# Optimization experiments

Measured on AMD Instinct MI355X. Metric: run time of the kernel, lower is better.

## Reference

```python
import jax, jax.numpy as jnp
import numpy as np

EPS = 1e-6

def _ln(x, g, b):
    m = jnp.mean(x, -1, keepdims=True)
    v = jnp.mean((x - m) ** 2, -1, keepdims=True)
    return (x - m) * jax.lax.rsqrt(v + 1e-5) * g + b

def _mha(qin, kin, vin, wq, bq, wk, bk, wv, bv, wo, bo, nh=8):
    B, T, D = qin.shape
    S = kin.shape[1]
    dh = D // nh
    q = (qin @ wq + bq).reshape(B, T, nh, dh)
    k = (kin @ wk + bk).reshape(B, S, nh, dh)
    v = (vin @ wv + bv).reshape(B, S, nh, dh)
    a = jax.nn.softmax(jnp.einsum('bthd,bshd->bhts', q, k) / np.float32(np.sqrt(dh)), -1)
    o = jnp.einsum('bhts,bshd->bthd', a, v).reshape(B, T, D)
    return o @ wo + bo

def _sinu_pe(pos, num_feats=128, temperature=20.0):
    # pos: [..., 2] (x, y); returns [..., 2*num_feats] ordered (y-feats, x-feats)
    dim_t = temperature ** ((2 * (jnp.arange(num_feats) // 2)) / num_feats)
    e = pos[..., None] * (2 * np.pi) / dim_t  # [..., 2, F]
    e = jnp.stack([jnp.sin(e[..., 0::2]), jnp.cos(e[..., 1::2])], -1).reshape(e.shape)
    return jnp.concatenate([e[..., 1, :], e[..., 0, :]], -1)

def _spatial36(b1, b2, sizes):
    # b1, b2: [B, Q, 4]; sizes: [B, 2] = (h, w). UPT-style 18 feats + log -> 36.
    h = sizes[:, 0:1]; w = sizes[:, 1:2]
    c1x = (b1[..., 0] + b1[..., 2]) / 2; c1y = (b1[..., 1] + b1[..., 3]) / 2
    c2x = (b2[..., 0] + b2[..., 2]) / 2; c2y = (b2[..., 1] + b2[..., 3]) / 2
    w1 = b1[..., 2] - b1[..., 0]; h1 = b1[..., 3] - b1[..., 1]
    w2 = b2[..., 2] - b2[..., 0]; h2 = b2[..., 3] - b2[..., 1]
    a1 = w1 * h1; a2 = w2 * h2
    dx = jnp.abs(c2x - c1x) / (w1 + EPS)
    dy = jnp.abs(c2y - c1y) / (h1 + EPS)
    ix = jnp.clip(jnp.minimum(b1[..., 2], b2[..., 2]) - jnp.maximum(b1[..., 0], b2[..., 0]), 0)
    iy = jnp.clip(jnp.minimum(b1[..., 3], b2[..., 3]) - jnp.maximum(b1[..., 1], b2[..., 1]), 0)
    inter = ix * iy
    iou = inter / (a1 + a2 - inter + EPS)
    f = jnp.stack([c1x / w, c1y / h, c2x / w, c2y / h, w1 / w, h1 / h, w2 / w, h2 / h,
                   a1 / (h * w), a2 / (h * w), a2 / (a1 + EPS), w1 / (h1 + EPS), w2 / (h2 + EPS), iou,
                   (c2x > c1x) * dx, (c2x < c1x) * dx, (c2y > c1y) * dy, (c2y < c1y) * dy], -1)
    return jnp.concatenate([f, jnp.log(f + EPS)], -1)

def _forward(boxes, embeds, image_sizes, pose, line, sw1, sb1, sw2, sb2, sw3, sb3, bw, bb, pw, pb, lw, lb, enc_pe_w, enc_pe_b, enc_qkv_w, enc_qkv_b, enc_out_w, enc_out_b, enc_ff1_w, enc_ff1_b, enc_ff2_w, enc_ff2_b, enc_ln1_g, enc_ln1_b, enc_ln2_g, enc_ln2_b, dec_q_w, dec_q_b, dec_kv_w, dec_kv_b, dec_out_w, dec_out_b, dec_ff1_w, dec_ff1_b, dec_ff2_w, dec_ff2_b, dec_ln1_g, dec_ln1_b, dec_ln2_g, dec_ln2_b, fc1_w, fc1_b, fc2_w, fc2_b, mln1_g, mln1_b, mln2_g, mln2_b, m1_w, m1_b, m2_w, m2_b, labels, nh):
    B, N, _ = boxes.shape
    # static human-object pairing (x != y) & (x < nh)
    xg, yg = np.meshgrid(np.arange(N), np.arange(N), indexing='ij')
    keep = (xg != yg) & (xg < nh)
    xk = jnp.asarray(xg[keep]); yk = jnp.asarray(yg[keep])  # [P]
    # line features: adaptive-avg-pool(1,1) + 1x1 conv == spatial mean + linear
    line_feat = jnp.mean(line, axis=(2, 3)) @ lw + lb  # [B, 256]
    # spatial head on all N*N ordered pairs, then gather kept pairs
    xa = jnp.asarray(xg.reshape(-1)); ya = jnp.asarray(yg.reshape(-1))
    f36 = _spatial36(boxes[:, xa], boxes[:, ya], image_sizes)  # [B, N*N, 36]
    s = jax.nn.relu(f36 @ sw1 + sb1)
    s = jax.nn.relu(s @ sw2 + sb2)
    s = jax.nn.relu(s @ sw3 + sb3)
    spa = s.reshape(B, N, N, -1)[:, xk, yk]  # [B, P, R]
    # box sinusoidal positional encodings (cat of centre-PE and wh-PE)
    whwh = image_sizes[:, jnp.array([1, 0, 1, 0])][:, None]  # [B,1,4]
    bxn = boxes / whwh
    ctr = (bxn[..., :2] + bxn[..., 2:]) / 2
    whb = bxn[..., 2:] - bxn[..., :2]
    box_pe = jnp.concatenate([_sinu_pe(ctr), _sinu_pe(whb)], -1)  # [B, N, 512]
    # 2-layer transformer encoder over instance tokens (pos added to q,k)
    posx = box_pe @ enc_pe_w + enc_pe_b
    x = embeds
    for i in range(enc_qkv_w.shape[0]):
        wq, wk_, wv = jnp.split(enc_qkv_w[i], 3, axis=1)
        bq, bk_, bv = jnp.split(enc_qkv_b[i], 3)
        qk = x + posx
        att = _mha(qk, qk, x, wq, bq, wk_, bk_, wv, bv, enc_out_w[i], enc_out_b[i])
        x = _ln(x + att, enc_ln1_g[i], enc_ln1_b[i])
        ff = jax.nn.relu(x @ enc_ff1_w[i] + enc_ff1_b[i]) @ enc_ff2_w[i] + enc_ff2_b[i]
        x = _ln(x + ff, enc_ln2_g[i], enc_ln2_b[i])
    # pair gather + human/object positional embeds (box PE projected + line feature)
    pe_h = box_pe[:, xk] @ bw + bb + line_feat[:, None, :]
    pe_o = box_pe[:, yk] @ bw + bb + line_feat[:, None, :]
    h = x[:, xk]; o = x[:, yk]  # [B, P, 256]
    pose_ctx = pose @ pw + pb  # [B, M, 256]
    # HO refine decoder: cross-attention from pair tokens to pose tokens
    for l in range(dec_q_w.shape[0]):
        wk_, wv = jnp.split(dec_kv_w[l], 2, axis=1)
        bk_, bv = jnp.split(dec_kv_b[l], 2)
        def _layer(feat, pe):
            att = _mha(feat + pe, pose_ctx, pose_ctx, dec_q_w[l], dec_q_b[l], wk_, bk_, wv, bv, dec_out_w[l], dec_out_b[l])
            feat = _ln(feat + att, dec_ln1_g[l], dec_ln1_b[l])
            ff = jax.nn.relu(feat @ dec_ff1_w[l] + dec_ff1_b[l]) @ dec_ff2_w[l] + dec_ff2_b[l]
            return _ln(feat + ff, dec_ln2_g[l], dec_ln2_b[l])
        h = _layer(h, pe_h)
        o = _layer(o, pe_o)
    # multi-modal fusion
    ho = jnp.concatenate([h, o], -1)  # [B, P, 512]
    ho = _ln(ho @ fc1_w + fc1_b, mln1_g, mln1_b)
    sp = _ln(spa @ fc2_w + fc2_b, mln2_g, mln2_b)
    z = jax.nn.relu(jnp.concatenate([ho, sp], -1))
    z = jax.nn.relu(z @ m1_w + m1_b)
    z = jax.nn.relu(z @ m2_w + m2_b)
    return z  # [B, P, 256] HOI query features

def setup_inputs() -> dict:
    key = jax.random.key(0)
    ks = iter(jax.random.split(key, 80))
    B, N, NH, M, HH, WW = 16, 128, 32, 64, 8, 8
    W = 0.05
    def rn(shape, s=1.0):
        return jax.random.normal(next(ks), shape, dtype=jnp.float32) * s
    def ru(shape):
        return jax.random.uniform(next(ks), shape, dtype=jnp.float32)
    sizes = 800.0 + 480.0 * ru((B, 2))  # (h, w)
    wh = sizes[:, jnp.array([1, 0])]
    xy = ru((B, N, 2)) * wh[:, None] * 0.7
    bwh = ru((B, N, 2)) * wh[:, None] * 0.25 + 4.0
    boxes = jnp.concatenate([xy, xy + bwh], -1)
    labels = jnp.concatenate([jnp.zeros((B, NH), jnp.int32), jax.random.randint(next(ks), (B, N - NH), 1, 81, dtype=jnp.int32)], -1)
    return dict(
        boxes=boxes, embeds=rn((B, N, 256)), image_sizes=sizes, pose=rn((B, M, 768)), line=rn((B, 2048, HH, WW)),
        sw1=rn((36, 128), W), sb1=jnp.zeros((128,)), sw2=rn((128, 256), W), sb2=jnp.zeros((256,)), sw3=rn((256, 256), W), sb3=jnp.zeros((256,)),
        bw=rn((512, 256), W), bb=jnp.zeros((256,)), pw=rn((768, 256), W), pb=jnp.zeros((256,)), lw=rn((2048, 256), W), lb=jnp.zeros((256,)),
        enc_pe_w=rn((512, 256), W), enc_pe_b=jnp.zeros((256,)),
        enc_qkv_w=rn((2, 256, 768), W), enc_qkv_b=jnp.zeros((2, 768)), enc_out_w=rn((2, 256, 256), W), enc_out_b=jnp.zeros((2, 256)),
        enc_ff1_w=rn((2, 256, 1024), W), enc_ff1_b=jnp.zeros((2, 1024)), enc_ff2_w=rn((2, 1024, 256), W), enc_ff2_b=jnp.zeros((2, 256)),
        enc_ln1_g=jnp.ones((2, 256)), enc_ln1_b=jnp.zeros((2, 256)), enc_ln2_g=jnp.ones((2, 256)), enc_ln2_b=jnp.zeros((2, 256)),
        dec_q_w=rn((2, 256, 256), W), dec_q_b=jnp.zeros((2, 256)), dec_kv_w=rn((2, 256, 512), W), dec_kv_b=jnp.zeros((2, 512)),
        dec_out_w=rn((2, 256, 256), W), dec_out_b=jnp.zeros((2, 256)),
        dec_ff1_w=rn((2, 256, 1024), W), dec_ff1_b=jnp.zeros((2, 1024)), dec_ff2_w=rn((2, 1024, 256), W), dec_ff2_b=jnp.zeros((2, 256)),
        dec_ln1_g=jnp.ones((2, 256)), dec_ln1_b=jnp.zeros((2, 256)), dec_ln2_g=jnp.ones((2, 256)), dec_ln2_b=jnp.zeros((2, 256)),
        fc1_w=rn((512, 256), W), fc1_b=jnp.zeros((256,)), fc2_w=rn((256, 256), W), fc2_b=jnp.zeros((256,)),
        mln1_g=jnp.ones((256,)), mln1_b=jnp.zeros((256,)), mln2_g=jnp.ones((256,)), mln2_b=jnp.zeros((256,)),
        m1_w=rn((512, 384), W), m1_b=jnp.zeros((384,)), m2_w=rn((384, 256), W), m2_b=jnp.zeros((256,)),
        labels=labels, nh=NH)

def reference(boxes, embeds, image_sizes, pose, line, sw1, sb1, sw2, sb2, sw3, sb3, bw, bb, pw, pb, lw, lb, enc_pe_w, enc_pe_b, enc_qkv_w, enc_qkv_b, enc_out_w, enc_out_b, enc_ff1_w, enc_ff1_b, enc_ff2_w, enc_ff2_b, enc_ln1_g, enc_ln1_b, enc_ln2_g, enc_ln2_b, dec_q_w, dec_q_b, dec_kv_w, dec_kv_b, dec_out_w, dec_out_b, dec_ff1_w, dec_ff1_b, dec_ff2_w, dec_ff2_b, dec_ln1_g, dec_ln1_b, dec_ln2_g, dec_ln2_b, fc1_w, fc1_b, fc2_w, fc2_b, mln1_g, mln1_b, mln2_g, mln2_b, m1_w, m1_b, m2_w, m2_b, labels, nh):
    return _forward(boxes, embeds, image_sizes, pose, line, sw1, sb1, sw2, sb2, sw3, sb3, bw, bb, pw, pb, lw, lb, enc_pe_w, enc_pe_b, enc_qkv_w, enc_qkv_b, enc_out_w, enc_out_b, enc_ff1_w, enc_ff1_b, enc_ff2_w, enc_ff2_b, enc_ln1_g, enc_ln1_b, enc_ln2_g, enc_ln2_b, dec_q_w, dec_q_b, dec_kv_w, dec_kv_b, dec_out_w, dec_out_b, dec_ff1_w, dec_ff1_b, dec_ff2_w, dec_ff2_b, dec_ln1_g, dec_ln1_b, dec_ln2_g, dec_ln2_b, fc1_w, fc1_b, fc2_w, fc2_b, mln1_g, mln1_b, mln2_g, mln2_b, m1_w, m1_b, m2_w, m2_b, labels, nh)
```

## Files before the change

kernel.cpp:

```cpp
#include <hip/hip_runtime.h>
#include <stdint.h>

static constexpr int B      = 16;
static constexpr int N      = 128;
static constexpr int P      = 4064;
static constexpr int MPOSE  = 64;
static constexpr int64_t BN = (int64_t)B * N;
static constexpr int64_t BP = (int64_t)B * P;

#define TWO_PI 6.283185307179586f
#define QSCALE 0.17677669529663687f

typedef __attribute__((ext_vector_type(4))) float f32x4;
typedef __attribute__((ext_vector_type(8))) short bf16x8;
typedef __attribute__((ext_vector_type(8))) unsigned short u16x8;
typedef __attribute__((ext_vector_type(4))) unsigned short u16x4;

__device__ __forceinline__ unsigned short f2bf(float f) {
    union { float f; unsigned u; } v; v.f = f;
    unsigned r = (v.u + 0x7fffu + ((v.u >> 16) & 1u)) >> 16;
    return (unsigned short)r;
}
__device__ __forceinline__ float bf2f(unsigned short u) {
    union { unsigned u; float f; } v; v.u = (unsigned)u << 16;
    return v.f;
}
__device__ __forceinline__ void pair_xy(int p, int& x, int& y) {
    x = p / 127;
    int r = p - x * 127;
    y = (r < x) ? r : r + 1;
}
__device__ __forceinline__ int xcd_swz(int orig, int nwg) {
    int q = nwg >> 3, r = nwg & 7;
    int xcd = orig & 7, idx = orig >> 3;
// ... 3 lines not shown
    __builtin_amdgcn_global_load_lds(
        (const __attribute__((address_space(1))) void*)g,
        (__attribute__((address_space(3))) void*)l, 16, 0, 0);
}

struct WDesc { const float* src; int64_t dstOff; int K, Nn, Kpad, blockStart; };
struct WTable { WDesc d[29]; int nDesc; };

__global__ __launch_bounds__(256) void wprep_all_k(WTable t, unsigned short* __restrict__ wt)
{
    __shared__ float s[32][33];
    int bid = blockIdx.x;
    int di = 0;
    for (int i = 1; i < t.nDesc; ++i) if (t.d[i].blockStart <= bid) di = i;
    const WDesc& d = t.d[di];
    int lbid = bid - d.blockStart;
    int kTiles = d.Kpad >> 5;
    int k0 = (lbid % kTiles) * 32, n0 = (lbid / kTiles) * 32;
    int tx = threadIdx.x & 31, ty = threadIdx.x >> 5;
#pragma unroll
    for (int i = 0; i < 4; ++i) {
        int k = k0 + ty + i * 8;
        s[ty + i * 8][tx] = (k < d.K) ? d.src[(int64_t)k * d.Nn + n0 + tx] : 0.f;
    }
    __syncthreads();
    unsigned short* dst = wt + d.dstOff;
#pragma unroll
    for (int i = 0; i < 4; ++i) {
        int n = n0 + ty + i * 8;
        dst[(int64_t)n * d.Kpad + k0 + tx] = f2bf(s[tx][ty + i * 8]);
    }
}

template <bool RELU_OUT>
__global__ __launch_bounds__(256) void bgemm_k(
    const float* __restrict__ A, const float* __restrict__ A2, int lda,
    const unsigned short* __restrict__ Bt, int ldk,
    const float* __restrict__ bias,
    const float* __restrict__ Cadd, int addLd,
    const float* __restrict__ lfp,
    float* __restrict__ C, int ldc,
    int kSteps)
{
    __shared__ unsigned short As[128][40];
    __shared__ unsigned short Bs[128][40];
    const int tid  = threadIdx.x;
    const int lane = tid & 63;
    const int wave = tid >> 6;
    const int wr = wave >> 1, wc = wave & 1;
    const int row0 = blockIdx.y * 128, col0 = blockIdx.x * 128;
    const int l15 = lane & 15, l4 = lane >> 4;
    const int sr = tid >> 1;
    const int sh = (tid & 1) * 16;

    f32x4 acc[4][4] = {};

    for (int ks = 0; ks < kSteps; ++ks) {
        const int k0 = ks * 32;
        {
            const int64_t off = (int64_t)(row0 + sr) * lda + k0 + sh;
            const float* ap = A + off;
            float v[16];
#pragma unroll
            for (int i = 0; i < 4; ++i) {
                float4 tv = ((const float4*)ap)[i];
                v[i*4+0] = tv.x; v[i*4+1] = tv.y; v[i*4+2] = tv.z; v[i*4+3] = tv.w;
            }
            if (A2) {
                const float* ap2 = A2 + off;
#pragma unroll
                for (int i = 0; i < 4; ++i) {
                    float4 tv = ((const float4*)ap2)[i];
                    v[i*4+0] += tv.x; v[i*4+1] += tv.y; v[i*4+2] += tv.z; v[i*4+3] += tv.w;
                }
            }
            u16x8 p0, p1;
#pragma unroll
            for (int j = 0; j < 8; ++j) { p0[j] = f2bf(v[j]); p1[j] = f2bf(v[8 + j]); }
            *(u16x8*)&As[sr][sh]     = p0;
            *(u16x8*)&As[sr][sh + 8] = p1;
        }
        {
            const unsigned short* bp = Bt + (int64_t)(col0 + sr) * ldk + k0 + sh;
            *(u16x8*)&Bs[sr][sh]     = *(const u16x8*)bp;
            *(u16x8*)&Bs[sr][sh + 8] = *(const u16x8*)(bp + 8);
        }
        __syncthreads();
        bf16x8 af[4], bfr[4];
#pragma unroll
        for (int f = 0; f < 4; ++f) {
            af[f]  = *(const bf16x8*)&As[wr * 64 + f * 16 + l15][l4 * 8];
            bfr[f] = *(const bf16x8*)&Bs[wc * 64 + f * 16 + l15][l4 * 8];
        }
#pragma unroll
        for (int i = 0; i < 4; ++i)
#pragma unroll
            for (int j = 0; j < 4; ++j)
                acc[i][j] = __builtin_amdgcn_mfma_f32_16x16x32_bf16(af[i], bfr[j], acc[i][j], 0, 0, 0);
        __syncthreads();
    }
#pragma unroll
    for (int i = 0; i < 4; ++i) {
        int rb = row0 + wr * 64 + i * 16 + l4 * 4;
#pragma unroll
        for (int j = 0; j < 4; ++j) {
            int c = col0 + wc * 64 + j * 16 + l15;
            float bv = bias ? bias[c] : 0.f;
#pragma unroll
            for (int e = 0; e < 4; ++e) {
                int r = rb + e;
                float vv = acc[i][j][e] + bv;
                if (Cadd && c < addLd) vv += Cadd[(int64_t)r * addLd + c];
                if (lfp) vv += lfp[(r >> 7) * 256 + c];
                if (RELU_OUT) vv = fmaxf(vv, 0.f);
                C[(int64_t)r * ldc + c] = vv;
            }
        }
    }
}

static void bgemm(hipStream_t st,
                  const float* A, const float* A2, int lda,
                  const unsigned short* Bt, int ldk, const float* bias,
                  const float* Cadd, int addLd, const float* lfp,
                  float* C, int ldc, int M, int Ncols, int K, bool reluOut)
{
    dim3 g(Ncols / 128, M / 128), b(256);
    if (reluOut) bgemm_k<true><<<g,b,0,st>>>(A,A2,lda,Bt,ldk,bias,Cadd,addLd,lfp,C,ldc,K/32);
    else         bgemm_k<false><<<g,b,0,st>>>(A,A2,lda,Bt,ldk,bias,Cadd,addLd,lfp,C,ldc,K/32);
}

__global__ __launch_bounds__(256) void tgemm_k(
    const float* __restrict__ A, int lda,
    const unsigned short* __restrict__ Bt, int ldk,
    const float* __restrict__ bias,
    const float* __restrict__ res,
    const float* __restrict__ g, const float* __restrict__ be,
    float* __restrict__ C, int kSteps)
{
    __shared__ unsigned short As[64][40];
    __shared__ unsigned short Bs[256][40];
    __shared__ float partS[64][4], partQ[64][4];
    __shared__ float statM[64], statI[64];
    const int tid = threadIdx.x;
    const int lane = tid & 63, w = tid >> 6;
    const int l15 = lane & 15, l4 = lane >> 4;
    const int row0 = blockIdx.x * 64;
    const int sra = tid >> 2, sha = (tid & 3) * 8;

    f32x4 acc[4][4] = {};
    for (int ks = 0; ks < kSteps; ++ks) {
        int k0 = ks * 32;
        {
            const float* ap = A + (int64_t)(row0 + sra) * lda + k0 + sha;
            float4 t0 = ((const float4*)ap)[0];
            float4 t1 = ((const float4*)ap)[1];
            u16x8 p;
            p[0]=f2bf(t0.x); p[1]=f2bf(t0.y); p[2]=f2bf(t0.z); p[3]=f2bf(t0.w);
            p[4]=f2bf(t1.x); p[5]=f2bf(t1.y); p[6]=f2bf(t1.z); p[7]=f2bf(t1.w);
            *(u16x8*)&As[sra][sha] = p;
        }
        {
            const unsigned short* bp = Bt + (int64_t)tid * ldk + k0;
#pragma unroll
            for (int q = 0; q < 4; ++q)
                *(u16x8*)&Bs[tid][q * 8] = *(const u16x8*)(bp + q * 8);
        }
        __syncthreads();
        bf16x8 af[4], bfr[4];
#pragma unroll
        for (int f = 0; f < 4; ++f) {
            af[f]  = *(const bf16x8*)&As[f * 16 + l15][l4 * 8];
            bfr[f] = *(const bf16x8*)&Bs[w * 64 + f * 16 + l15][l4 * 8];
        }
#pragma unroll
        for (int i = 0; i < 4; ++i)
#pragma unroll
            for (int j = 0; j < 4; ++j)
                acc[i][j] = __builtin_amdgcn_mfma_f32_16x16x32_bf16(af[i], bfr[j], acc[i][j], 0, 0, 0);
        __syncthreads();
// ... 24 lines not shown
        }
    }
    if (l15 == 0) {
#pragma unroll
        for (int i = 0; i < 4; ++i)
#pragma unroll
        for (int e = 0; e < 4; ++e) {
            int r = i * 16 + l4 * 4 + e;
            partS[r][w] = ps[i][e];
            partQ[r][w] = pq[i][e];
        }
    }
    __syncthreads();
    if (tid < 64) {
        float s = partS[tid][0] + partS[tid][1] + partS[tid][2] + partS[tid][3];
        float q = partQ[tid][0] + partQ[tid][1] + partQ[tid][2] + partQ[tid][3];
        float m = s * (1.f/256.f);
        float var = q * (1.f/256.f) - m * m;
        statM[tid] = m;
        statI[tid] = rsqrtf(var + 1e-5f);
    }
    __syncthreads();
#pragma unroll
    for (int i = 0; i < 4; ++i)
#pragma unroll
    for (int j = 0; j < 4; ++j) {
        int c = w * 64 + j * 16 + l15;
#pragma unroll
        for (int e = 0; e < 4; ++e) {
            int r = i * 16 + l4 * 4 + e;
            C[(int64_t)(row0 + r) * 256 + c] = (acc[i][j][e] - statM[r]) * statI[r] * g[c] + be[c];
        }
    }
}

template <bool RELU_OUT, bool OUT_BF16>
__global__ __launch_bounds__(256) void hgemm_k(
    const unsigned short* __restrict__ A, int lda,
    const unsigned short* __restrict__ Bt, int ldk,
    const float* __restrict__ bias,
    void* __restrict__ Cv, int ldc,
    int kSteps, int nx)
{
    __shared__ unsigned short As[128][32];
    __shared__ unsigned short Bs[128][32];
    const int tid  = threadIdx.x;
    const int lane = tid & 63;
    const int wave = tid >> 6;
    const int wr = wave >> 1, wc = wave & 1;
    const int wgid = xcd_swz(blockIdx.x, gridDim.x);
    const int row0 = (wgid / nx) * 128, col0 = (wgid % nx) * 128;
    const int l15 = lane & 15, l4 = lane >> 4;
    const int srow = lane >> 2;
    const int scol = (lane & 3) * 8;

    f32x4 acc[4][4] = {};

    for (int ks = 0; ks < kSteps; ++ks) {
        const int k0 = ks * 32;
#pragma unroll
        for (int i = 0; i < 2; ++i) {
            int seg = wave * 2 + i;
            int r = seg * 16 + srow;
            gld16(A  + (int64_t)(row0 + r) * lda + k0 + scol, &As[seg * 16][0]);
            gld16(Bt + (int64_t)(col0 + r) * ldk + k0 + scol, &Bs[seg * 16][0]);
        }
        __syncthreads();
        bf16x8 af[4], bfr[4];
#pragma unroll
        for (int f = 0; f < 4; ++f) {
            af[f]  = *(const bf16x8*)&As[wr * 64 + f * 16 + l15][l4 * 8];
            bfr[f] = *(const bf16x8*)&Bs[wc * 64 + f * 16 + l15][l4 * 8];
        }
#pragma unroll
        for (int i = 0; i < 4; ++i)
#pragma unroll
            for (int j = 0; j < 4; ++j)
                acc[i][j] = __builtin_amdgcn_mfma_f32_16x16x32_bf16(af[i], bfr[j], acc[i][j], 0, 0, 0);
        __syncthreads();
    }
#pragma unroll
    for (int i = 0; i < 4; ++i) {
        int rb = row0 + wr * 64 + i * 16 + l4 * 4;
#pragma unroll
        for (int j = 0; j < 4; ++j) {
            int c = col0 + wc * 64 + j * 16 + l15;
            float bv = bias ? bias[c] : 0.f;
#pragma unroll
            for (int e = 0; e < 4; ++e) {
                int64_t off = (int64_t)(rb + e) * ldc + c;
// ... 224 lines not shown
#pragma unroll 4
    for (int k = 0; k < 256; ++k) acc += lmb[k] * lwp[(int64_t)k * 256];
    red[cc][jj] = acc;
    __syncthreads();
    if (cc == 0) {
        float s = lb[j];
#pragma unroll
        for (int i = 0; i < 8; ++i) s += red[i][jj];
        lf[b * 256 + j] = s;
    }
}

__global__ __launch_bounds__(512) void boxpe_k(
    const float* __restrict__ boxes, const float* __restrict__ sizes, float* __restrict__ boxpe)
{
    int row = blockIdx.x;
    int b = row >> 7;
    int i = threadIdx.x;
    const float* bx = boxes + (int64_t)row * 4;
    float h = sizes[b * 2 + 0], w = sizes[b * 2 + 1];
    float x0 = bx[0] / w, y0 = bx[1] / h, x1 = bx[2] / w, y1 = bx[3] / h;
    int seg = i >> 7, j = i & 127, k = j >> 1;
    float val;
    switch (seg) {
        case 0: val = (y0 + y1) * 0.5f; break;
        case 1: val = (x0 + x1) * 0.5f; break;
        case 2: val = (y1 - y0); break;
        default: val = (x1 - x0); break;
    }
    float dimt = exp2f((float)k * (4.321928094887362f / 64.f));
    float arg = val * TWO_PI / dimt;
    boxpe[(int64_t)row * 512 + i] = (j & 1) ? cosf(arg) : sinf(arg);
}

__global__ __launch_bounds__(128) void enc_attn_k(
    const float* __restrict__ qkv, float* __restrict__ outp)
{
    int b = blockIdx.x >> 3, hd = blockIdx.x & 7;
    __shared__ float kl[128][32];
    __shared__ float vl[128][32];
    int tid = threadIdx.x;
    for (int i = tid; i < 128 * 32; i += 128) {
        int s = i >> 5, j = i & 31;
        const float* rp = qkv + ((int64_t)(b * 128 + s)) * 768 + hd * 32 + j;
        kl[s][j] = rp[256];
        vl[s][j] = rp[512];
    }
    __syncthreads();
    int t = tid;
    const float* qp = qkv + ((int64_t)(b * 128 + t)) * 768 + hd * 32;
    float qr[32];
#pragma unroll
    for (int j = 0; j < 32; ++j) qr[j] = qp[j] * QSCALE;
    float m = -1e30f, l = 0.f;
    for (int s = 0; s < 128; ++s) {
        float d = 0.f;
#pragma unroll
        for (int j = 0; j < 32; ++j) d += qr[j] * kl[s][j];
        float mn = fmaxf(m, d);
        l = l * __expf(m - mn) + __expf(d - mn);
        m = mn;
    }
    float acc[32] = {};
    for (int s = 0; s < 128; ++s) {
        float d = 0.f;
#pragma unroll
        for (int j = 0; j < 32; ++j) d += qr[j] * kl[s][j];
        float wgt = __expf(d - m);
#pragma unroll
        for (int j = 0; j < 32; ++j) acc[j] += wgt * vl[s][j];
    }
    float linv = 1.f / l;
    float* op = outp + ((int64_t)(b * 128 + t)) * 256 + hd * 32;
#pragma unroll
    for (int j = 0; j < 32; ++j) op[j] = acc[j] * linv;
}

__global__ __launch_bounds__(256) void dec_attn_k(
    const float* __restrict__ q, const float* __restrict__ kv,
    float* __restrict__ outp, int rows, int rpb)
{
    int hd = blockIdx.y;
    int r0 = blockIdx.x * 256;
    __shared__ float kl[2][64][32];
    __shared__ float vl[2][64][32];
    int tid = threadIdx.x;
    int b0 = r0 / rpb;
    int b1 = (r0 + 255) / rpb;
    if (b1 >= B) b1 = B - 1;
    for (int i = tid; i < 64 * 32; i += 256) {
        int s = i >> 5, j = i & 31;
        int64_t off0 = ((int64_t)(b0 * MPOSE + s)) * 512 + hd * 32 + j;
        int64_t off1 = ((int64_t)(b1 * MPOSE + s)) * 512 + hd * 32 + j;
        kl[0][s][j] = kv[off0];
        vl[0][s][j] = kv[off0 + 256];
        kl[1][s][j] = kv[off1];
        vl[1][s][j] = kv[off1 + 256];
    }
    __syncthreads();
    int r = r0 + tid;
    if (r >= rows) return;
    int which = (r / rpb == b0) ? 0 : 1;
    int64_t qoff = (int64_t)r * 256 + hd * 32;
    float qr[32];
#pragma unroll
    for (int j = 0; j < 32; ++j) qr[j] = q[qoff + j] * QSCALE;
    float m = -1e30f, l = 0.f;
    for (int s = 0; s < 64; ++s) {
        float d = 0.f;
#pragma unroll
        for (int j = 0; j < 32; ++j) d += qr[j] * kl[which][s][j];
        float mn = fmaxf(m, d);
        l = l * __expf(m - mn) + __expf(d - mn);
        m = mn;
    }
    float acc[32] = {};
    for (int s = 0; s < 64; ++s) {
        float d = 0.f;
#pragma unroll
        for (int j = 0; j < 32; ++j) d += qr[j] * kl[which][s][j];
        float wgt = __expf(d - m);
#pragma unroll
        for (int j = 0; j < 32; ++j) acc[j] += wgt * vl[which][s][j];
    }
    float linv = 1.f / l;
#pragma unroll
    for (int j = 0; j < 32; ++j) outp[qoff + j] = acc[j] * linv;
}

static constexpr int64_t WT_QKV  = 0;
static constexpr int64_t WT_EOUT = WT_QKV  + 2*196608;
static constexpr int64_t WT_EFF1 = WT_EOUT + 2*65536;
static constexpr int64_t WT_EFF2 = WT_EFF1 + 2*262144;
static constexpr int64_t WT_DQ   = WT_EFF2 + 2*262144;
static constexpr int64_t WT_DKV  = WT_DQ   + 2*65536;
static constexpr int64_t WT_DOUT = WT_DKV  + 2*131072;
static constexpr int64_t WT_DFF1 = WT_DOUT + 2*65536;
static constexpr int64_t WT_DFF2 = WT_DFF1 + 2*262144;
static constexpr int64_t WT_SW1  = WT_DFF2 + 2*262144;
static constexpr int64_t WT_SW2  = WT_SW1 + 8192;
static constexpr int64_t WT_SW3  = WT_SW2 + 32768;
static constexpr int64_t WT_BW   = WT_SW3 + 65536;
static constexpr int64_t WT_PW   = WT_BW  + 131072;
static constexpr int64_t WT_EPE  = WT_PW  + 196608;
static constexpr int64_t WT_FC1  = WT_EPE + 131072;
static constexpr int64_t WT_FC2  = WT_FC1 + 131072;
static constexpr int64_t WT_M1   = WT_FC2 + 65536;
static constexpr int64_t WT_M2   = WT_M1  + 196608;
static constexpr int64_t WT_TOTAL = WT_M2 + 98304;

extern "C" void kernel_launch(void* const* d_in, const int* in_sizes, int n_in,
                              void* d_out, int out_size, void* d_ws, size_t ws_size,
                              hipStream_t stream)
{
    (void)in_sizes; (void)n_in; (void)out_size;
    const float* boxes     = (const float*)d_in[0];
    const float* embeds    = (const float*)d_in[1];
    const float* sizes     = (const float*)d_in[2];
    const float* pose      = (const float*)d_in[3];
    const float* line      = (const float*)d_in[4];
    const float* sw1 = (const float*)d_in[5];  const float* sb1 = (const float*)d_in[6];
    const float* sw2 = (const float*)d_in[7];  const float* sb2 = (const float*)d_in[8];
    const float* sw3 = (const float*)d_in[9];  const float* sb3 = (const float*)d_in[10];
    const float* bw  = (const float*)d_in[11]; const float* bb  = (const float*)d_in[12];
    const float* pw  = (const float*)d_in[13]; const float* pb  = (const float*)d_in[14];
    const float* lw  = (const float*)d_in[15]; const float* lb  = (const float*)d_in[16];
    const float* enc_pe_w  = (const float*)d_in[17]; const float* enc_pe_b = (const float*)d_in[18];
    const float* enc_qkv_w = (const float*)d_in[19]; const float* enc_qkv_b = (const float*)d_in[20];
    const float* enc_out_w = (const float*)d_in[21]; const float* enc_out_b = (const float*)d_in[22];
    const float* enc_ff1_w = (const float*)d_in[23]; const float* enc_ff1_b = (const float*)d_in[24];
    const float* enc_ff2_w = (const float*)d_in[25]; const float* enc_ff2_b = (const float*)d_in[26];
    const float* enc_ln1_g = (const float*)d_in[27]; const float* enc_ln1_b = (const float*)d_in[28];
    const float* enc_ln2_g = (const float*)d_in[29]; const float* enc_ln2_b = (const float*)d_in[30];
    const float* dec_q_w   = (const float*)d_in[31]; const float* dec_q_b  = (const float*)d_in[32];
    const float* dec_kv_w  = (const float*)d_in[33]; const float* dec_kv_b = (const float*)d_in[34];
    const float* dec_out_w = (const float*)d_in[35]; const float* dec_out_b = (const float*)d_in[36];
    const float* dec_ff1_w = (const float*)d_in[37]; const float* dec_ff1_b = (const float*)d_in[38];
    const float* dec_ff2_w = (const float*)d_in[39]; const float* dec_ff2_b = (const float*)d_in[40];
    const float* dec_ln1_g = (const float*)d_in[41]; const float* dec_ln1_b = (const float*)d_in[42];
    const float* dec_ln2_g = (const float*)d_in[43]; const float* dec_ln2_b = (const float*)d_in[44];
    const float* fc1_w = (const float*)d_in[45]; const float* fc1_b = (const float*)d_in[46];
    const float* fc2_w = (const float*)d_in[47]; const float* fc2_b = (const float*)d_in[48];
// ... 45 lines not shown
            add(dec_q_w   + (int64_t)i*65536,  WT_DQ   + i*65536,  256, 256, 256);
            add(dec_kv_w  + (int64_t)i*131072, WT_DKV  + i*131072, 256, 512, 256);
            add(dec_out_w + (int64_t)i*65536,  WT_DOUT + i*65536,  256, 256, 256);
            add(dec_ff1_w + (int64_t)i*262144, WT_DFF1 + i*262144, 256, 1024, 256);
            add(dec_ff2_w + (int64_t)i*262144, WT_DFF2 + i*262144, 1024, 256, 1024);
        }
        add(sw1, WT_SW1, 36, 128, 64);
        add(sw2, WT_SW2, 128, 256, 128);
        add(sw3, WT_SW3, 256, 256, 256);
        add(bw,  WT_BW,  512, 256, 512);
        add(pw,  WT_PW,  768, 256, 768);
        add(enc_pe_w, WT_EPE, 512, 256, 512);
        add(fc1_w,             WT_FC1,         256, 256, 256);
        add(fc1_w + 256 * 256, WT_FC1 + 65536, 256, 256, 256);
        add(fc2_w, WT_FC2, 256, 256, 256);
        add(m1_w, WT_M1, 512, 384, 512);
        add(m2_w, WT_M2, 384, 256, 384);
        T.nDesc = nd;
        wprep_all_k<<<bs, 256, 0, stream>>>(T, wt);
    }

    line_mean_k<<<8192, 256, 0, stream>>>(line, lm);
    line_proj_k<<<dim3(8, B), 256, 0, stream>>>(lm, lw, lb, lf);
    boxpe_k<<<(int)BN, 512, 0, stream>>>(boxes, sizes, boxpe);
    bgemm(stream, boxpe, nullptr, 512, wt + WT_EPE, 512, enc_pe_b, nullptr, 0, nullptr, posx, 256, (int)BN, 256, 512, false);
    bgemm(stream, boxpe, nullptr, 512, wt + WT_BW,  512, bb,       nullptr, 0, lf,      bpw_, 256, (int)BN, 256, 512, false);
    bgemm(stream, pose,  nullptr, 768, wt + WT_PW,  768, pb,       nullptr, 0, nullptr, pctx, 256, B*MPOSE, 256, 768, false);
    for (int l = 0; l < 2; ++l)
        bgemm(stream, pctx, nullptr, 256, wt + WT_DKV + l*131072, 256, dec_kv_b + (int64_t)l*512,
              nullptr, 0, nullptr, kv0 + (int64_t)l*524288, 512, B*MPOSE, 512, 256, false);
    bgemm(stream, posx, nullptr, 256, wt + WT_QKV,          256, nullptr, nullptr, 0, nullptr, pqk0, 512, (int)BN, 512, 256, false);
    bgemm(stream, posx, nullptr, 256, wt + WT_QKV + 196608, 256, nullptr, nullptr, 0, nullptr, pqk1, 512, (int)BN, 512, 256, false);

    for (int i = 0; i < 2; ++i) {
        const float* xin = (i == 0) ? embeds : x_;
        const float* pqk = (i == 0) ? pqk0 : pqk1;
        const unsigned short* Wq = wt + WT_QKV + (int64_t)i * 196608;
        bgemm(stream, xin, nullptr, 256, Wq, 256, enc_qkv_b + (int64_t)i*768, pqk, 512, nullptr,
              e_qkv, 768, (int)BN, 768, 256, false);
        enc_attn_k<<<B * 8, 128, 0, stream>>>(e_qkv, e_t);
        tgemm_k<<<(int)(BN / 64), 256, 0, stream>>>(e_t, 256, wt + WT_EOUT + (int64_t)i*65536, 256,
            enc_out_b + i*256, xin, enc_ln1_g + i*256, enc_ln1_b + i*256, x_, 8);
        bgemm(stream, x_, nullptr, 256, wt + WT_EFF1 + (int64_t)i*262144, 256, enc_ff1_b + i*1024,
              nullptr, 0, nullptr, e_ff, 1024, (int)BN, 1024, 256, true);
        tgemm_k<<<(int)(BN / 64), 256, 0, stream>>>(e_ff, 1024, wt + WT_EFF2 + (int64_t)i*262144, 1024,
            enc_ff2_b + i*256, x_, enc_ln2_g + i*256, enc_ln2_b + i*256, x_, 32);
    }

    for (int l = 0; l < 2; ++l) {
        bgemm(stream, x_, bpw_, 256, wt + WT_DQ + (int64_t)l*65536, 256, dec_q_b + l*256,
              nullptr, 0, nullptr, e_t, 256, (int)BN, 256, 256, false);
        dec_attn_k<<<dim3((int)(BN / 256), 8), 256, 0, stream>>>(e_t, kv0 + (int64_t)l*524288, e_qkv, (int)BN, N);
        tgemm_k<<<(int)(BN / 64), 256, 0, stream>>>(e_qkv, 256, wt + WT_DOUT + (int64_t)l*65536, 256,
            dec_out_b + l*256, x_, dec_ln1_g + l*256, dec_ln1_b + l*256, x_, 8);
        bgemm(stream, x_, nullptr, 256, wt + WT_DFF1 + (int64_t)l*262144, 256, dec_ff1_b + l*1024,
              nullptr, 0, nullptr, e_ff, 1024, (int)BN, 1024, 256, true);
        tgemm_k<<<(int)(BN / 64), 256, 0, stream>>>(e_ff, 1024, wt + WT_DFF2 + (int64_t)l*262144, 1024,
            dec_ff2_b + l*256, x_, dec_ln2_g + l*256, dec_ln2_b + l*256, x_, 32);
    }
    float* UV = kv0;
    bgemm(stream, x_, nullptr, 256, wt + WT_FC1, 256, nullptr, nullptr, 0, nullptr, UV, 512, (int)BN, 512, 256, false);

    for (int64_t c0 = 0; c0 < BP; c0 += rc) {
        int rows = (int)((BP - c0 < rc) ? (BP - c0) : rc);
        unsigned short* t3 = (unsigned short*)arena;
        unsigned short* zb = t3 + (int64_t)rc * 256;
        unsigned short* z2 = zb + (int64_t)rc * 512;

        spa_k<<<rows / 128, 256, 0, stream>>>(boxes, sizes,
            wt + WT_SW1, sb1, wt + WT_SW2, sb2, t3, (int)c0);
        hgemm_k<true,true><<<2 * (rows / 128), 256, 0, stream>>>(
            t3, 256, wt + WT_SW3, 256, sb3, z2, 256, 8, 2);
        hgemm_k<false,true><<<2 * (rows / 128), 256, 0, stream>>>(
            z2, 256, wt + WT_FC2, 256, fc2_b, t3, 256, 8, 2);
        zprep_k<<<rows / 4, 256, 0, stream>>>(UV, fc1_b, t3, mln1_g, mln1_b, mln2_g, mln2_b,
                                              zb, (int)c0, rows);
        hgemm_k<true,true><<<3 * (rows / 128), 256, 0, stream>>>(
            zb, 512, wt + WT_M1, 512, m1_b, z2, 384, 16, 3);
        hgemm_k<true,false><<<2 * (rows / 128), 256, 0, stream>>>(
            z2, 384, wt + WT_M2, 384, m2_b, out + c0 * 256, 256, 12, 2);
    }
}
```

Measured before the change: 913.5 us.

## Fuse encoder/decoder token stages into one cooperative persistent kernel

```diff
diff --git a/kernel.cpp b/kernel.cpp
--- a/kernel.cpp
+++ b/kernel.cpp
@@ -1,5 +1,8 @@
 #include <hip/hip_runtime.h>
+#include <hip/hip_cooperative_groups.h>
 #include <stdint.h>
+
+namespace cg = cooperative_groups;
 
 static constexpr int B      = 16;
 static constexpr int N      = 128;
@@ -69,29 +72,32 @@
     }
 }
 
+static constexpr int SMEM_BYTES = 32768;
+
 template <bool RELU_OUT>
-__global__ __launch_bounds__(256) void bgemm_k(
+__device__ __forceinline__ void d_bgemm(char* sm, int bid,
     const float* __restrict__ A, const float* __restrict__ A2, int lda,
     const unsigned short* __restrict__ Bt, int ldk,
     const float* __restrict__ bias,
     const float* __restrict__ Cadd, int addLd,
     const float* __restrict__ lfp,
     float* __restrict__ C, int ldc,
-    int kSteps)
-{
-    __shared__ unsigned short As[128][40];
-    __shared__ unsigned short Bs[128][40];
+    int kSteps, int nx, int nblocks)
+{
+    if (bid >= nblocks) return;
+    typedef unsigned short row40[40];
+    row40* As = (row40*)sm;
+    row40* Bs = (row40*)(sm + 10240);
     const int tid  = threadIdx.x;
     const int lane = tid & 63;
     const int wave = tid >> 6;
     const int wr = wave >> 1, wc = wave & 1;
-    const int row0 = blockIdx.y * 128, col0 = blockIdx.x * 128;
+    const int row0 = (bid / nx) * 128, col0 = (bid % nx) * 128;
     const int l15 = lane & 15, l4 = lane >> 4;
     const int sr = tid >> 1;
     const int sh = (tid & 1) * 16;
 
     f32x4 acc[4][4] = {};
-
     for (int ks = 0; ks < kSteps; ++ks) {
         const int k0 = ks * 32;
         {
@@ -156,18 +162,7 @@
     }
 }
 
-static void bgemm(hipStream_t st,
-                  const float* A, const float* A2, int lda,
-                  const unsigned short* Bt, int ldk, const float* bias,
-                  const float* Cadd, int addLd, const float* lfp,
-                  float* C, int ldc, int M, int Ncols, int K, bool reluOut)
-{
-    dim3 g(Ncols / 128, M / 128), b(256);
-    if (reluOut) bgemm_k<true><<<g,b,0,st>>>(A,A2,lda,Bt,ldk,bias,Cadd,addLd,lfp,C,ldc,K/32);
-    else         bgemm_k<false><<<g,b,0,st>>>(A,A2,lda,Bt,ldk,bias,Cadd,addLd,lfp,C,ldc,K/32);
-}
-
-__global__ __launch_bounds__(256) void tgemm_k(
+__device__ __forceinline__ void d_tgemm(char* sm, int bid,
     const float* __restrict__ A, int lda,
     const unsigned short* __restrict__ Bt, int ldk,
     const float* __restrict__ bias,
@@ -175,14 +170,18 @@
     const float* __restrict__ g, const float* __restrict__ be,
     float* __restrict__ C, int kSteps)
 {
-    __shared__ unsigned short As[64][40];
-    __shared__ unsigned short Bs[256][40];
-    __shared__ float partS[64][4], partQ[64][4];
-    __shared__ float statM[64], statI[64];
+    if (bid >= 32) return;
+    typedef unsigned short rowA[40];
+    rowA* As = (rowA*)sm;
+    rowA* Bs = (rowA*)(sm + 5120);
+    float (*partS)[4] = (float(*)[4])(sm + 25600);
+    float (*partQ)[4] = (float(*)[4])(sm + 26624);
+    float* statM = (float*)(sm + 27648);
+    float* statI = (float*)(sm + 27904);
     const int tid = threadIdx.x;
     const int lane = tid & 63, w = tid >> 6;
     const int l15 = lane & 15, l4 = lane >> 4;
-    const int row0 = blockIdx.x * 64;
+    const int row0 = bid * 64;
     const int sra = tid >> 2, sha = (tid & 3) * 8;
 
     f32x4 acc[4][4] = {};
@@ -273,6 +272,226 @@
             C[(int64_t)(row0 + r) * 256 + c] = (acc[i][j][e] - statM[r]) * statI[r] * g[c] + be[c];
         }
     }
+    __syncthreads();
+}
+
+__device__ __forceinline__ void d_eattn(char* sm, int bid,
+    const float* __restrict__ qkv, float* __restrict__ outp)
+{
+    if (bid >= 128) return;
+    int b = bid >> 3, hd = bid & 7;
+    float (*kl)[32] = (float(*)[32])sm;
+    float (*vl)[32] = (float(*)[32])(sm + 16384);
+    int tid = threadIdx.x;
+    for (int i = tid; i < 128 * 32; i += 256) {
+        int s = i >> 5, j = i & 31;
+        const float* rp = qkv + ((int64_t)(b * 128 + s)) * 768 + hd * 32 + j;
+        kl[s][j] = rp[256];
+        vl[s][j] = rp[512];
+    }
+    __syncthreads();
+    if (tid < 128) {
+        int t = tid;
+        const float* qp = qkv + ((int64_t)(b * 128 + t)) * 768 + hd * 32;
+        float qr[32];
+#pragma unroll
+        for (int j = 0; j < 32; ++j) qr[j] = qp[j] * QSCALE;
+        float m = -1e30f, l = 0.f;
+        for (int s = 0; s < 128; ++s) {
+            float d = 0.f;
+#pragma unroll
+            for (int j = 0; j < 32; ++j) d += qr[j] * kl[s][j];
+            float mn = fmaxf(m, d);
+            l = l * __expf(m - mn) + __expf(d - mn);
+            m = mn;
+        }
+        float acc[32] = {};
+        for (int s = 0; s < 128; ++s) {
+            float d = 0.f;
+#pragma unroll
+            for (int j = 0; j < 32; ++j) d += qr[j] * kl[s][j];
+            float wgt = __expf(d - m);
+#pragma unroll
+            for (int j = 0; j < 32; ++j) acc[j] += wgt * vl[s][j];
+        }
+        float linv = 1.f / l;
+        float* op = outp + ((int64_t)(b * 128 + t)) * 256 + hd * 32;
+#pragma unroll
+        for (int j = 0; j < 32; ++j) op[j] = acc[j] * linv;
+    }
+    __syncthreads();
+}
+
+__device__ __forceinline__ void d_dattn(char* sm, int bid,
+    const float* __restrict__ q, const float* __restrict__ kv,
+    float* __restrict__ outp)
+{
+    if (bid >= 64) return;
+    int rblk = bid >> 3, hd = bid & 7;
+    int r0 = rblk * 256;
+    float (*kl)[32] = (float(*)[32])sm;
+    float (*vl)[32] = (float(*)[32])(sm + 16384);
+    int tid = threadIdx.x;
+    int b0 = r0 / N;
+    int b1 = b0 + 1;
+    for (int i = tid; i < 64 * 32; i += 256) {
+        int s = i >> 5, j = i & 31;
+        int64_t off0 = ((int64_t)(b0 * MPOSE + s)) * 512 + hd * 32 + j;
+        int64_t off1 = ((int64_t)(b1 * MPOSE + s)) * 512 + hd * 32 + j;
+        kl[s][j]      = kv[off0];
+        vl[s][j]      = kv[off0 + 256];
+        kl[64 + s][j] = kv[off1];
+        vl[64 + s][j] = kv[off1 + 256];
+    }
+    __syncthreads();
+    int r = r0 + tid;
+    int which = (tid < 128) ? 0 : 1;
+    {
+        int64_t qoff = (int64_t)r * 256 + hd * 32;
+        float qr[32];
+#pragma unroll
+        for (int j = 0; j < 32; ++j) qr[j] = q[qoff + j] * QSCALE;
+        float m = -1e30f, l = 0.f;
+        for (int s = 0; s < 64; ++s) {
+            float d = 0.f;
+#pragma unroll
+            for (int j = 0; j < 32; ++j) d += qr[j] * kl[which * 64 + s][j];
+            float mn = fmaxf(m, d);
+            l = l * __expf(m - mn) + __expf(d - mn);
+            m = mn;
+        }
+        float acc[32] = {};
+        for (int s = 0; s < 64; ++s) {
+            float d = 0.f;
+#pragma unroll
+            for (int j = 0; j < 32; ++j) d += qr[j] * kl[which * 64 + s][j];
+            float wgt = __expf(d - m);
+#pragma unroll
+            for (int j = 0; j < 32; ++j) acc[j] += wgt * vl[which * 64 + s][j];
+        }
+        float linv = 1.f / l;
+#pragma unroll
+        for (int j = 0; j < 32; ++j) outp[qoff + j] = acc[j] * linv;
+    }
+    __syncthreads();
+}
+
+template <bool RELU_OUT>
+__global__ __launch_bounds__(256) void bgemm1_k(
+    const float* A, const float* A2, int lda,
+    const unsigned short* Bt, int ldk, const float* bias,
+    const float* Cadd, int addLd, const float* lfp,
+    float* C, int ldc, int kSteps, int nx, int nblocks)
+{
+    __shared__ char sm[SMEM_BYTES];
+    d_bgemm<RELU_OUT>(sm, blockIdx.x, A, A2, lda, Bt, ldk, bias, Cadd, addLd, lfp, C, ldc, kSteps, nx, nblocks);
+}
+
+__global__ __launch_bounds__(256) void tgemm1_k(
+    const float* A, int lda, const unsigned short* Bt, int ldk,
+    const float* bias, const float* res, const float* g, const float* be,
+    float* C, int kSteps)
+{
+    __shared__ char sm[SMEM_BYTES];
+    d_tgemm(sm, blockIdx.x, A, lda, Bt, ldk, bias, res, g, be, C, kSteps);
+}
+
+__global__ __launch_bounds__(256) void eattn_k(const float* qkv, float* outp)
+{
+    __shared__ char sm[SMEM_BYTES];
+    d_eattn(sm, blockIdx.x, qkv, outp);
+}
+
+__global__ __launch_bounds__(256) void dattn_k(const float* q, const float* kv, float* outp)
+{
+    __shared__ char sm[SMEM_BYTES];
+    d_dattn(sm, blockIdx.x, q, kv, outp);
+}
+
+static void bgemm(hipStream_t st,
+                  const float* A, const float* A2, int lda,
+                  const unsigned short* Bt, int ldk, const float* bias,
+                  const float* Cadd, int addLd, const float* lfp,
+                  float* C, int ldc, int M, int Ncols, int K, bool reluOut)
+{
+    int nx = Ncols / 128, nb = nx * (M / 128);
+    if (reluOut) bgemm1_k<true><<<nb,256,0,st>>>(A,A2,lda,Bt,ldk,bias,Cadd,addLd,lfp,C,ldc,K/32,nx,nb);
+    else         bgemm1_k<false><<<nb,256,0,st>>>(A,A2,lda,Bt,ldk,bias,Cadd,addLd,lfp,C,ldc,K/32,nx,nb);
+}
+
+static constexpr int64_t WT_QKV  = 0;
+static constexpr int64_t WT_EOUT = WT_QKV  + 2*196608;
+static constexpr int64_t WT_EFF1 = WT_EOUT + 2*65536;
+static constexpr int64_t WT_EFF2 = WT_EFF1 + 2*262144;
+static constexpr int64_t WT_DQ   = WT_EFF2 + 2*262144;
+static constexpr int64_t WT_DKV  = WT_DQ   + 2*65536;
+static constexpr int64_t WT_DOUT = WT_DKV  + 2*131072;
+static constexpr int64_t WT_DFF1 = WT_DOUT + 2*65536;
+static constexpr int64_t WT_DFF2 = WT_DFF1 + 2*262144;
+static constexpr int64_t WT_SW1  = WT_DFF2 + 2*262144;
+static constexpr int64_t WT_SW2  = WT_SW1 + 8192;
+static constexpr int64_t WT_SW3  = WT_SW2 + 32768;
+static constexpr int64_t WT_BW   = WT_SW3 + 65536;
+static constexpr int64_t WT_PW   = WT_BW  + 131072;
+static constexpr int64_t WT_EPE  = WT_PW  + 196608;
+static constexpr int64_t WT_FC1  = WT_EPE + 131072;
+static constexpr int64_t WT_FC2  = WT_FC1 + 131072;
+static constexpr int64_t WT_M1   = WT_FC2 + 65536;
+static constexpr int64_t WT_M2   = WT_M1  + 196608;
+static constexpr int64_t WT_TOTAL = WT_M2 + 98304;
+
+struct TokArgs {
+    const float *embeds, *bpw, *pqk0, *pqk1, *kv0;
+    float *x, *eqkv, *et, *eff, *UV;
+    const unsigned short *wt;
+    const float *eqkv_b, *eout_b, *eff1_b, *eff2_b;
+    const float *eln1_g, *eln1_b, *eln2_g, *eln2_b;
+    const float *dq_b, *dout_b, *dff1_b, *dff2_b;
+    const float *dln1_g, *dln1_b, *dln2_g, *dln2_b;
+};
+
+__global__ __launch_bounds__(256) void megatok_k(TokArgs a)
+{
+    __shared__ char sm[SMEM_BYTES];
+    cg::grid_group grid = cg::this_grid();
+    const int bid = blockIdx.x;
+    for (int i = 0; i < 2; ++i) {
+        const float* xin = i ? (const float*)a.x : a.embeds;
+        const float* pqk = i ? a.pqk1 : a.pqk0;
+        const unsigned short* Wq = a.wt + WT_QKV + (int64_t)i * 196608;
+        d_bgemm<false>(sm, bid, xin, nullptr, 256, Wq, 256, a.eqkv_b + i*768, pqk, 512, nullptr,
+                       a.eqkv, 768, 8, 6, 96);
+        grid.sync();
+        d_eattn(sm, bid, a.eqkv, a.et);
+        grid.sync();
+        d_tgemm(sm, bid, a.et, 256, a.wt + WT_EOUT + (int64_t)i*65536, 256,
+                a.eout_b + i*256, xin, a.eln1_g + i*256, a.eln1_b + i*256, a.x, 8);
+        grid.sync();
+        d_bgemm<true>(sm, bid, a.x, nullptr, 256, a.wt + WT_EFF1 + (int64_t)i*262144, 256,
+                      a.eff1_b + i*1024, nullptr, 0, nullptr, a.eff, 1024, 8, 8, 128);
+        grid.sync();
+        d_tgemm(sm, bid, a.eff, 1024, a.wt + WT_EFF2 + (int64_t)i*262144, 1024,
+                a.eff2_b + i*256, a.x, a.eln2_g + i*256, a.eln2_b + i*256, a.x, 32);
+        grid.sync();
+    }
+    for (int l = 0; l < 2; ++l) {
+        d_bgemm<false>(sm, bid, a.x, a.bpw, 256, a.wt + WT_DQ + (int64_t)l*65536, 256,
+                       a.dq_b + l*256, nullptr, 0, nullptr, a.et, 256, 8, 2, 32);
+        grid.sync();
+        d_dattn(sm, bid, a.et, a.kv0 + (int64_t)l*524288, a.eqkv);
+        grid.sync();
+        d_tgemm(sm, bid, a.eqkv, 256, a.wt + WT_DOUT + (int64_t)l*65536, 256,
+                a.dout_b + l*256, a.x, a.dln1_g + l*256, a.dln1_b + l*256, a.x, 8);
+        grid.sync();
+        d_bgemm<true>(sm, bid, a.x, nullptr, 256, a.wt + WT_DFF1 + (int64_t)l*262144, 256,
+                      a.dff1_b + l*1024, nullptr, 0, nullptr, a.eff, 1024, 8, 8, 128);
+        grid.sync();
+        d_tgemm(sm, bid, a.eff, 1024, a.wt + WT_DFF2 + (int64_t)l*262144, 1024,
+                a.dff2_b + l*256, a.x, a.dln2_g + l*256, a.dln2_b + l*256, a.x, 32);
+        grid.sync();
+    }
+    d_bgemm<false>(sm, bid, a.x, nullptr, 256, a.wt + WT_FC1, 256, nullptr, nullptr, 0, nullptr,
+                   a.UV, 512, 8, 4, 64);
 }
 
 template <bool RELU_OUT, bool OUT_BF16>
@@ -296,7 +515,6 @@
     const int scol = (lane & 3) * 8;
 
     f32x4 acc[4][4] = {};
-
     for (int ks = 0; ks < kSteps; ++ks) {
         const int k0 = ks * 32;
 #pragma unroll
@@ -587,122 +805,6 @@
     float arg = val * TWO_PI / dimt;
     boxpe[(int64_t)row * 512 + i] = (j & 1) ? cosf(arg) : sinf(arg);
 }
-
-__global__ __launch_bounds__(128) void enc_attn_k(
-    const float* __restrict__ qkv, float* __restrict__ outp)
-{
-    int b = blockIdx.x >> 3, hd = blockIdx.x & 7;
-    __shared__ float kl[128][32];
-    __shared__ float vl[128][32];
-    int tid = threadIdx.x;
-    for (int i = tid; i < 128 * 32; i += 128) {
-        int s = i >> 5, j = i & 31;
-        const float* rp = qkv + ((int64_t)(b * 128 + s)) * 768 + hd * 32 + j;
-        kl[s][j] = rp[256];
-        vl[s][j] = rp[512];
-    }
-    __syncthreads();
-    int t = tid;
-    const float* qp = qkv + ((int64_t)(b * 128 + t)) * 768 + hd * 32;
-    float qr[32];
-#pragma unroll
-    for (int j = 0; j < 32; ++j) qr[j] = qp[j] * QSCALE;
-    float m = -1e30f, l = 0.f;
-    for (int s = 0; s < 128; ++s) {
-        float d = 0.f;
-#pragma unroll
-        for (int j = 0; j < 32; ++j) d += qr[j] * kl[s][j];
-        float mn = fmaxf(m, d);
-        l = l * __expf(m - mn) + __expf(d - mn);
-        m = mn;
-    }
-    float acc[32] = {};
-    for (int s = 0; s < 128; ++s) {
-        float d = 0.f;
-#pragma unroll
-        for (int j = 0; j < 32; ++j) d += qr[j] * kl[s][j];
-        float wgt = __expf(d - m);
-#pragma unroll
-        for (int j = 0; j < 32; ++j) acc[j] += wgt * vl[s][j];
-    }
-    float linv = 1.f / l;
-    float* op = outp + ((int64_t)(b * 128 + t)) * 256 + hd * 32;
-#pragma unroll
-    for (int j = 0; j < 32; ++j) op[j] = acc[j] * linv;
-}
-
-__global__ __launch_bounds__(256) void dec_attn_k(
-    const float* __restrict__ q, const float* __restrict__ kv,
-    float* __restrict__ outp, int rows, int rpb)
-{
-    int hd = blockIdx.y;
-    int r0 = blockIdx.x * 256;
-    __shared__ float kl[2][64][32];
-    __shared__ float vl[2][64][32];
-    int tid = threadIdx.x;
-    int b0 = r0 / rpb;
-    int b1 = (r0 + 255) / rpb;
-    if (b1 >= B) b1 = B - 1;
-    for (int i = tid; i < 64 * 32; i += 256) {
-        int s = i >> 5, j = i & 31;
-        int64_t off0 = ((int64_t)(b0 * MPOSE + s)) * 512 + hd * 32 + j;
-        int64_t off1 = ((int64_t)(b1 * MPOSE + s)) * 512 + hd * 32 + j;
-        kl[0][s][j] = kv[off0];
-        vl[0][s][j] = kv[off0 + 256];
-        kl[1][s][j] = kv[off1];
-        vl[1][s][j] = kv[off1 + 256];
-    }
-    __syncthreads();
-    int r = r0 + tid;
-    if (r >= rows) return;
-    int which = (r / rpb == b0) ? 0 : 1;
-    int64_t qoff = (int64_t)r * 256 + hd * 32;
-    float qr[32];
-#pragma unroll
-    for (int j = 0; j < 32; ++j) qr[j] = q[qoff + j] * QSCALE;
-    float m = -1e30f, l = 0.f;
-    for (int s = 0; s < 64; ++s) {
-        float d = 0.f;
-#pragma unroll
-        for (int j = 0; j < 32; ++j) d += qr[j] * kl[which][s][j];
-        float mn = fmaxf(m, d);
-        l = l * __expf(m - mn) + __expf(d - mn);
-        m = mn;
-    }
-    float acc[32] = {};
-    for (int s = 0; s < 64; ++s) {
-        float d = 0.f;
-#pragma unroll
-        for (int j = 0; j < 32; ++j) d += qr[j] * kl[which][s][j];
-        float wgt = __expf(d - m);
-#pragma unroll
-        for (int j = 0; j < 32; ++j) acc[j] += wgt * vl[which][s][j];
-    }
-    float linv = 1.f / l;
-#pragma unroll
-    for (int j = 0; j < 32; ++j) outp[qoff + j] = acc[j] * linv;
-}
-
-static constexpr int64_t WT_QKV  = 0;
-static constexpr int64_t WT_EOUT = WT_QKV  + 2*196608;
-static constexpr int64_t WT_EFF1 = WT_EOUT + 2*65536;
-static constexpr int64_t WT_EFF2 = WT_EFF1 + 2*262144;
-static constexpr int64_t WT_DQ   = WT_EFF2 + 2*262144;
-static constexpr int64_t WT_DKV  = WT_DQ   + 2*65536;
-static constexpr int64_t WT_DOUT = WT_DKV  + 2*131072;
-static constexpr int64_t WT_DFF1 = WT_DOUT + 2*65536;
-static constexpr int64_t WT_DFF2 = WT_DFF1 + 2*262144;
-static constexpr int64_t WT_SW1  = WT_DFF2 + 2*262144;
-static constexpr int64_t WT_SW2  = WT_SW1 + 8192;
-static constexpr int64_t WT_SW3  = WT_SW2 + 32768;
-static constexpr int64_t WT_BW   = WT_SW3 + 65536;
-static constexpr int64_t WT_PW   = WT_BW  + 131072;
-static constexpr int64_t WT_EPE  = WT_PW  + 196608;
-static constexpr int64_t WT_FC1  = WT_EPE + 131072;
-static constexpr int64_t WT_FC2  = WT_FC1 + 131072;
-static constexpr int64_t WT_M1   = WT_FC2 + 65536;
-static constexpr int64_t WT_M2   = WT_M1  + 196608;
-static constexpr int64_t WT_TOTAL = WT_M2 + 98304;
 
 extern "C" void kernel_launch(void* const* d_in, const int* in_sizes, int n_in,
                               void* d_out, int out_size, void* d_ws, size_t ws_size,
@@ -814,34 +916,48 @@
     bgemm(stream, posx, nullptr, 256, wt + WT_QKV,          256, nullptr, nullptr, 0, nullptr, pqk0, 512, (int)BN, 512, 256, false);
     bgemm(stream, posx, nullptr, 256, wt + WT_QKV + 196608, 256, nullptr, nullptr, 0, nullptr, pqk1, 512, (int)BN, 512, 256, false);
 
-    for (int i = 0; i < 2; ++i) {
-        const float* xin = (i == 0) ? embeds : x_;
-        const float* pqk = (i == 0) ? pqk0 : pqk1;
-        const unsigned short* Wq = wt + WT_QKV + (int64_t)i * 196608;
-        bgemm(stream, xin, nullptr, 256, Wq, 256, enc_qkv_b + (int64_t)i*768, pqk, 512, nullptr,
-              e_qkv, 768, (int)BN, 768, 256, false);
-        enc_attn_k<<<B * 8, 128, 0, stream>>>(e_qkv, e_t);
-        tgemm_k<<<(int)(BN / 64), 256, 0, stream>>>(e_t, 256, wt + WT_EOUT + (int64_t)i*65536, 256,
-            enc_out_b + i*256, xin, enc_ln1_g + i*256, enc_ln1_b + i*256, x_, 8);
-        bgemm(stream, x_, nullptr, 256, wt + WT_EFF1 + (int64_t)i*262144, 256, enc_ff1_b + i*1024,
-              nullptr, 0, nullptr, e_ff, 1024, (int)BN, 1024, 256, true);
-        tgemm_k<<<(int)(BN / 64), 256, 0, stream>>>(e_ff, 1024, wt + WT_EFF2 + (int64_t)i*262144, 1024,
-            enc_ff2_b + i*256, x_, enc_ln2_g + i*256, enc_ln2_b + i*256, x_, 32);
-    }
-
-    for (int l = 0; l < 2; ++l) {
-        bgemm(stream, x_, bpw_, 256, wt + WT_DQ + (int64_t)l*65536, 256, dec_q_b + l*256,
-              nullptr, 0, nullptr, e_t, 256, (int)BN, 256, 256, false);
-        dec_attn_k<<<dim3((int)(BN / 256), 8), 256, 0, stream>>>(e_t, kv0 + (int64_t)l*524288, e_qkv, (int)BN, N);
-        tgemm_k<<<(int)(BN / 64), 256, 0, stream>>>(e_qkv, 256, wt + WT_DOUT + (int64_t)l*65536, 256,
-            dec_out_b + l*256, x_, dec_ln1_g + l*256, dec_ln1_b + l*256, x_, 8);
-        bgemm(stream, x_, nullptr, 256, wt + WT_DFF1 + (int64_t)l*262144, 256, dec_ff1_b + l*1024,
-              nullptr, 0, nullptr, e_ff, 1024, (int)BN, 1024, 256, true);
-        tgemm_k<<<(int)(BN / 64), 256, 0, stream>>>(e_ff, 1024, wt + WT_DFF2 + (int64_t)l*262144, 1024,
-            dec_ff2_b + l*256, x_, dec_ln2_g + l*256, dec_ln2_b + l*256, x_, 32);
-    }
     float* UV = kv0;
-    bgemm(stream, x_, nullptr, 256, wt + WT_FC1, 256, nullptr, nullptr, 0, nullptr, UV, 512, (int)BN, 512, 256, false);
+    {
+        TokArgs ta;
+        ta.embeds = embeds; ta.bpw = bpw_; ta.pqk0 = pqk0; ta.pqk1 = pqk1; ta.kv0 = kv0;
+        ta.x = x_; ta.eqkv = e_qkv; ta.et = e_t; ta.eff = e_ff; ta.UV = UV;
+        ta.wt = wt;
+        ta.eqkv_b = enc_qkv_b; ta.eout_b = enc_out_b; ta.eff1_b = enc_ff1_b; ta.eff2_b = enc_ff2_b;
+        ta.eln1_g = enc_ln1_g; ta.eln1_b = enc_ln1_b; ta.eln2_g = enc_ln2_g; ta.eln2_b = enc_ln2_b;
+        ta.dq_b = dec_q_b; ta.dout_b = dec_out_b; ta.dff1_b = dec_ff1_b; ta.dff2_b = dec_ff2_b;
+        ta.dln1_g = dec_ln1_g; ta.dln1_b = dec_ln1_b; ta.dln2_g = dec_ln2_g; ta.dln2_b = dec_ln2_b;
+        void* kargs[] = { &ta };
+        hipError_t err = hipLaunchCooperativeKernel((const void*)megatok_k,
+                                                    dim3(128), dim3(256), kargs, 0, stream);
+        if (err != hipSuccess) {
+            for (int i = 0; i < 2; ++i) {
+                const float* xin = i ? x_ : embeds;
+                const float* pqk = i ? pqk1 : pqk0;
+                const unsigned short* Wq = wt + WT_QKV + (int64_t)i * 196608;
+                bgemm(stream, xin, nullptr, 256, Wq, 256, enc_qkv_b + (int64_t)i*768, pqk, 512, nullptr,
+                      e_qkv, 768, (int)BN, 768, 256, false);
+                eattn_k<<<128, 256, 0, stream>>>(e_qkv, e_t);
+                tgemm1_k<<<32, 256, 0, stream>>>(e_t, 256, wt + WT_EOUT + (int64_t)i*65536, 256,
+                    enc_out_b + i*256, xin, enc_ln1_g + i*256, enc_ln1_b + i*256, x_, 8);
+                bgemm(stream, x_, nullptr, 256, wt + WT_EFF1 + (int64_t)i*262144, 256, enc_ff1_b + i*1024,
+                      nullptr, 0, nullptr, e_ff, 1024, (int)BN, 1024, 256, true);
+                tgemm1_k<<<32, 256, 0, stream>>>(e_ff, 1024, wt + WT_EFF2 + (int64_t)i*262144, 1024,
+                    enc_ff2_b + i*256, x_, enc_ln2_g + i*256, enc_ln2_b + i*256, x_, 32);
+            }
+            for (int l = 0; l < 2; ++l) {
+                bgemm(stream, x_, bpw_, 256, wt + WT_DQ + (int64_t)l*65536, 256, dec_q_b + l*256,
+                      nullptr, 0, nullptr, e_t, 256, (int)BN, 256, 256, false);
+                dattn_k<<<64, 256, 0, stream>>>(e_t, kv0 + (int64_t)l*524288, e_qkv);
+                tgemm1_k<<<32, 256, 0, stream>>>(e_qkv, 256, wt + WT_DOUT + (int64_t)l*65536, 256,
+                    dec_out_b + l*256, x_, dec_ln1_g + l*256, dec_ln1_b + l*256, x_, 8);
+                bgemm(stream, x_, nullptr, 256, wt + WT_DFF1 + (int64_t)l*262144, 256, dec_ff1_b + l*1024,
+                      nullptr, 0, nullptr, e_ff, 1024, (int)BN, 1024, 256, true);
+                tgemm1_k<<<32, 256, 0, stream>>>(e_ff, 1024, wt + WT_DFF2 + (int64_t)l*262144, 1024,
+                    dec_ff2_b + l*256, x_, dec_ln2_g + l*256, dec_ln2_b + l*256, x_, 32);
+            }
+            bgemm(stream, x_, nullptr, 256, wt + WT_FC1, 256, nullptr, nullptr, 0, nullptr, UV, 512, (int)BN, 512, 256, false);
+        }
+    }
 
     for (int64_t c0 = 0; c0 < BP; c0 += rc) {
         int rows = (int)((BP - c0 < rc) ? (BP - c0) : rc);
```

New measurement: 1.315 ms (median of 2 runs). 1.44x slower.
